# Optimization experiments

Measured on AMD Instinct MI355X. Metric: run time of the kernel, lower is better.

## Reference

```python
import jax, jax.numpy as jnp
import numpy as np

STRIPE = 8
EPS = 1e-5  # PyTorch BatchNorm default eps


def setup_inputs() -> dict:
    key = jax.random.key(0)
    ks = jax.random.split(key, 8)
    b, c, t, h, w = 4, 256, 8, 128, 64
    ic = c // 2  # inter_channels default = in_channels // 2
    scale = 0.02
    return {
        "x": jax.random.normal(ks[0], (b, c, t, h, w), jnp.float32),
        # 1x1 Conv3d weights are just channel-mixing matrices (out, in)
        "g_w": jax.random.normal(ks[1], (ic, c), jnp.float32) * scale,
        "g_b": jnp.zeros((ic,), jnp.float32),
        "theta_w": jax.random.normal(ks[2], (ic, c), jnp.float32) * scale,
        "theta_b": jnp.zeros((ic,), jnp.float32),
        "phi_w": jax.random.normal(ks[3], (ic, c), jnp.float32) * scale,
        "phi_b": jnp.zeros((ic,), jnp.float32),
        "W_w": jax.random.normal(ks[4], (c, ic), jnp.float32) * scale,
        "W_b": jnp.zeros((c,), jnp.float32),
        # BatchNorm3d (eval mode): original inits gamma=beta=0; use nonzero
        # gamma here so the reference output is non-trivial.
        "bn_gamma": jax.random.normal(ks[5], (c,), jnp.float32) * 0.1,
        "bn_beta": jax.random.normal(ks[6], (c,), jnp.float32) * 0.1,
        "bn_mean": jnp.zeros((c,), jnp.float32),
        "bn_var": jnp.ones((c,), jnp.float32),
    }


def reference(x, g_w, g_b, theta_w, theta_b, phi_w, phi_b,
              W_w, W_b, bn_gamma, bn_beta, bn_mean, bn_var):
    b, c, t, h, w = x.shape
    hs = h // STRIPE
    # stripe mean-pool: AdaptiveAvgPool2d(1) over each (hs, w) stripe region
    xr = x.reshape(b, c, t, STRIPE, hs, w)
    d = xr.mean(axis=(4, 5))                      # (b, c, t, stripe)
    S = t * STRIPE
    dn = d.reshape(b, c, S)                       # tokens: (b, c, S)
    # 1x1 conv3d projections == channel matmuls
    g = jnp.einsum('bcs,ic->bsi', dn, g_w) + g_b          # (b, S, ic)
    th = jnp.einsum('bcs,ic->bsi', dn, theta_w) + theta_b  # (b, S, ic)
    ph = jnp.einsum('bcs,ic->bsi', dn, phi_w) + phi_b      # (b, S, ic)
    # small self-attention over stripe tokens
    f = jnp.einsum('bsi,bri->bsr', th, ph)                 # (b, S, S)
    attn = jax.nn.softmax(f, axis=-1)                      # instance='soft'
    y = jnp.einsum('bsr,bri->bsi', attn, g)                # (b, S, ic)
    # output 1x1 conv + BatchNorm3d (eval mode, running stats)
    Wy = jnp.einsum('bsi,ci->bcs', y, W_w) + W_b[None, :, None]  # (b, c, S)
    inv = bn_gamma / jnp.sqrt(bn_var + EPS)
    Wy = (Wy - bn_mean[None, :, None]) * inv[None, :, None] + bn_beta[None, :, None]
    # broadcast each stripe value back over its (hs, w) region + residual
    Wy = Wy.reshape(b, c, t, STRIPE, 1, 1)
    z = (xr + Wy).reshape(b, c, t, h, w)
    return z
```

## Files before the change

### kernel.cpp

```cpp
#include <hip/hip_runtime.h>
#include <hip/hip_bf16.h>
#include <math.h>

#define B 4
#define C 256
#define T 8
#define H 128
#define WW 64
#define IC 128
#define S 64
#define NSTRIPE 8
#define HS 16
#define REGION 1024
#define EPS 1e-5f

__global__ void pool_kernel(const float* __restrict__ x, float* __restrict__ dn) {
    int sb = blockIdx.x;
    const float4* xr = (const float4*)(x + (size_t)sb * REGION);
    float4 v = xr[threadIdx.x];
    float sum = v.x + v.y + v.z + v.w;
    #pragma unroll
    for (int off = 32; off > 0; off >>= 1)
        sum += __shfl_down(sum, off, 64);
    __shared__ float ws[4];
    int wid = threadIdx.x >> 6;
    int lane = threadIdx.x & 63;
    if (lane == 0) ws[wid] = sum;
    __syncthreads();
    if (threadIdx.x == 0) {
        float tot = ws[0] + ws[1] + ws[2] + ws[3];
        dn[sb] = tot * (1.0f / (float)REGION);
    }
}

__global__ void proj_kernel(const float* __restrict__ dn,
                            const float* __restrict__ gw, const float* __restrict__ gb,
                            const float* __restrict__ tw, const float* __restrict__ tb,
                            const float* __restrict__ pw, const float* __restrict__ pb,
                            float* __restrict__ g, float* __restrict__ th,
                            float* __restrict__ ph) {
    int blk = blockIdx.x;
    int b = blk >> 6, s = blk & 63;
    __shared__ float dloc[C];
    for (int ch = threadIdx.x; ch < C; ch += blockDim.x)
        dloc[ch] = dn[(b * C + ch) * S + s];
    __syncthreads();
    int i = threadIdx.x;
    float ag = gb[i], at = tb[i], ap = pb[i];
    const float* gwr = gw + i * C;
    const float* twr = tw + i * C;
    const float* pwr = pw + i * C;
    for (int ch = 0; ch < C; ++ch) {
        float d = dloc[ch];
        ag = fmaf(d, gwr[ch], ag);
        at = fmaf(d, twr[ch], at);
        ap = fmaf(d, pwr[ch], ap);
    }
    size_t o = ((size_t)(b * S + s)) * IC + i;
    g[o] = ag; th[o] = at; ph[o] = ap;
}

__global__ void attn_kernel(const float* __restrict__ g,
                            const float* __restrict__ th,
                            const float* __restrict__ ph,
                            float* __restrict__ y) {
    int blk = blockIdx.x;
    int b = blk >> 6, s = blk & 63;
    __shared__ float p[S];
    __shared__ float thloc[IC];
    int tid = threadIdx.x;
    thloc[tid] = th[((size_t)(b * S + s)) * IC + tid];
    __syncthreads();
    if (tid < 64) {
        int r = tid;
        const float* phr = ph + ((size_t)(b * S + r)) * IC;
        float f = 0.0f;
        for (int i = 0; i < IC; ++i) f = fmaf(thloc[i], phr[i], f);
        float m = f;
        #pragma unroll
        for (int off = 32; off > 0; off >>= 1)
            m = fmaxf(m, __shfl_xor(m, off, 64));
        float e = __expf(f - m);
        float sum = e;
        #pragma unroll
        for (int off = 32; off > 0; off >>= 1)
            sum += __shfl_xor(sum, off, 64);
        p[r] = e / sum;
    }
    __syncthreads();
    int i = tid;
    float acc = 0.0f;
    for (int r = 0; r < S; ++r)
        acc = fmaf(p[r], g[((size_t)(b * S + r)) * IC + i], acc);
    y[((size_t)(b * S + s)) * IC + i] = acc;
}

__global__ void outproj_kernel(const float* __restrict__ y,
                               const float* __restrict__ Ww, const float* __restrict__ Wb,
                               const float* __restrict__ gamma, const float* __restrict__ beta,
                               const float* __restrict__ mean, const float* __restrict__ var,
                               float* __restrict__ wy) {
    int idx = blockIdx.x * blockDim.x + threadIdx.x;
    int s = idx & 63;
    int ch = (idx >> 6) & 255;
    int b = idx >> 14;
    const float* yr = y + ((size_t)(b * S + s)) * IC;
    const float* wr = Ww + (size_t)ch * IC;
    float acc = Wb[ch];
    for (int i = 0; i < IC; ++i) acc = fmaf(yr[i], wr[i], acc);
    float inv = gamma[ch] * rsqrtf(var[ch] + EPS);
    wy[idx] = (acc - mean[ch]) * inv + beta[ch];
}

__global__ void add_kernel(const float* __restrict__ x,
                           const float* __restrict__ wy,
                           float* __restrict__ out) {
    size_t f = (size_t)blockIdx.x * blockDim.x + threadIdx.x;
    const float4* x4 = (const float4*)x;
    float4* o4 = (float4*)out;
    float4 v = x4[f];
    float a = wy[f >> 8];
    v.x += a; v.y += a; v.z += a; v.w += a;
    o4[f] = v;
}

extern "C" void kernel_launch(void* const* d_in, const int* in_sizes, int n_in,
                              void* d_out, int out_size, void* d_ws, size_t ws_size,
                              hipStream_t stream) {
    const float* x       = (const float*)d_in[0];
    const float* g_w     = (const float*)d_in[1];
    const float* g_b     = (const float*)d_in[2];
    const float* theta_w = (const float*)d_in[3];
    const float* theta_b = (const float*)d_in[4];
    const float* phi_w   = (const float*)d_in[5];
    const float* phi_b   = (const float*)d_in[6];
    const float* W_w     = (const float*)d_in[7];
    const float* W_b     = (const float*)d_in[8];
    const float* bn_g    = (const float*)d_in[9];
    const float* bn_b    = (const float*)d_in[10];
    const float* bn_m    = (const float*)d_in[11];
    const float* bn_v    = (const float*)d_in[12];
    float* out = (float*)d_out;

    float* ws = (float*)d_ws;
    float* dn = ws;
    float* g  = dn + B * C * S;
    float* th = g  + B * S * IC;
    float* ph = th + B * S * IC;
    float* y  = ph + B * S * IC;
    float* wy = y  + B * S * IC;

    const int nRegions = B * C * T * NSTRIPE;
    pool_kernel<<<nRegions, 256, 0, stream>>>(x, dn);

    proj_kernel<<<B * S, IC, 0, stream>>>(dn, g_w, g_b, theta_w, theta_b,
                                          phi_w, phi_b, g, th, ph);

    attn_kernel<<<B * S, IC, 0, stream>>>(g, th, ph, y);

    outproj_kernel<<<(B * C * S) / 256, 256, 0, stream>>>(y, W_w, W_b,
                                                          bn_g, bn_b, bn_m, bn_v, wy);

    const size_t nVec4 = (size_t)B * C * T * H * WW / 4;
    add_kernel<<<(int)(nVec4 / 256), 256, 0, stream>>>(x, wy, out);
}
```

Measured before the change: 516.3 us.

## Transpose weights for coalesced projections, fuse attention with output projection

Adds a kernel that transposes the projection weights so that threads in the projection and output-projection loops read consecutive addresses. The pool kernel now reduces 16 regions per wave and writes the pooled tokens transposed, so the projection kernel can load them contiguously. The attention kernel computes scores with wave-parallel dot products and is fused with the output projection and BatchNorm, which removes one launch and the intermediate y buffer. The cost is an extra transpose launch on every call and fewer pool blocks; the large add pass is unchanged and likely dominates the runtime.

```diff
diff --git a/kernel.cpp b/kernel.cpp
--- a/kernel.cpp
+++ b/kernel.cpp
@@ -9,73 +9,111 @@
 #define WW 64
 #define IC 128
 #define S 64
-#define NSTRIPE 8
-#define HS 16
 #define REGION 1024
+#define NREGION 65536
 #define EPS 1e-5f
 
-__global__ void pool_kernel(const float* __restrict__ x, float* __restrict__ dn) {
-    int sb = blockIdx.x;
-    const float4* xr = (const float4*)(x + (size_t)sb * REGION);
-    float4 v = xr[threadIdx.x];
-    float sum = v.x + v.y + v.z + v.w;
-    #pragma unroll
-    for (int off = 32; off > 0; off >>= 1)
-        sum += __shfl_down(sum, off, 64);
-    __shared__ float ws[4];
-    int wid = threadIdx.x >> 6;
-    int lane = threadIdx.x & 63;
-    if (lane == 0) ws[wid] = sum;
-    __syncthreads();
-    if (threadIdx.x == 0) {
-        float tot = ws[0] + ws[1] + ws[2] + ws[3];
-        dn[sb] = tot * (1.0f / (float)REGION);
-    }
-}
-
-__global__ void proj_kernel(const float* __restrict__ dn,
-                            const float* __restrict__ gw, const float* __restrict__ gb,
-                            const float* __restrict__ tw, const float* __restrict__ tb,
-                            const float* __restrict__ pw, const float* __restrict__ pb,
+__global__ void transpose_kernel(const float* __restrict__ gw,
+                                 const float* __restrict__ tw,
+                                 const float* __restrict__ pw,
+                                 const float* __restrict__ Ww,
+                                 float* __restrict__ gwT, float* __restrict__ twT,
+                                 float* __restrict__ pwT, float* __restrict__ WwT) {
+    int t = blockIdx.x * blockDim.x + threadIdx.x;
+    int m = t >> 15;
+    int e = t & 32767;
+    if (m < 3) {
+        int ch = e >> 7, i = e & 127;
+        const float* src = (m == 0) ? gw : (m == 1) ? tw : pw;
+        float* dst = (m == 0) ? gwT : (m == 1) ? twT : pwT;
+        dst[e] = src[i * C + ch];
+    } else {
+        int i = e >> 8, ch = e & 255;
+        WwT[e] = Ww[ch * IC + i];
+    }
+}
+
+__global__ void pool_kernel(const float* __restrict__ x, float* __restrict__ dnT) {
+    int tid = threadIdx.x;
+    int lane = tid & 63;
+    int wgid = (blockIdx.x << 2) | (tid >> 6);
+    int r0 = wgid << 4;
+    for (int k = 0; k < 16; ++k) {
+        int r = r0 + k;
+        const float4* xr = (const float4*)(x + (size_t)r * REGION);
+        float4 a = xr[lane];
+        float4 b = xr[lane + 64];
+        float4 c = xr[lane + 128];
+        float4 d = xr[lane + 192];
+        float sum = (a.x + a.y + a.z + a.w) + (b.x + b.y + b.z + b.w)
+                  + (c.x + c.y + c.z + c.w) + (d.x + d.y + d.z + d.w);
+        #pragma unroll
+        for (int off = 32; off > 0; off >>= 1)
+            sum += __shfl_xor(sum, off, 64);
+        if (lane == 0) {
+            int idx = (r & 0xC000) | ((r & 63) << 8) | ((r >> 6) & 255);
+            dnT[idx] = sum * (1.0f / (float)REGION);
+        }
+    }
+}
+
+__global__ void proj_kernel(const float* __restrict__ dnT,
+                            const float* __restrict__ gwT, const float* __restrict__ gb,
+                            const float* __restrict__ twT, const float* __restrict__ tb,
+                            const float* __restrict__ pwT, const float* __restrict__ pb,
                             float* __restrict__ g, float* __restrict__ th,
                             float* __restrict__ ph) {
     int blk = blockIdx.x;
-    int b = blk >> 6, s = blk & 63;
     __shared__ float dloc[C];
-    for (int ch = threadIdx.x; ch < C; ch += blockDim.x)
-        dloc[ch] = dn[(b * C + ch) * S + s];
+    const float2* dr = (const float2*)(dnT + (size_t)blk * C);
+    ((float2*)dloc)[threadIdx.x] = dr[threadIdx.x];
     __syncthreads();
     int i = threadIdx.x;
     float ag = gb[i], at = tb[i], ap = pb[i];
-    const float* gwr = gw + i * C;
-    const float* twr = tw + i * C;
-    const float* pwr = pw + i * C;
+    #pragma unroll 4
     for (int ch = 0; ch < C; ++ch) {
         float d = dloc[ch];
-        ag = fmaf(d, gwr[ch], ag);
-        at = fmaf(d, twr[ch], at);
-        ap = fmaf(d, pwr[ch], ap);
-    }
-    size_t o = ((size_t)(b * S + s)) * IC + i;
+        int o = (ch << 7) + i;
+        ag = fmaf(d, gwT[o], ag);
+        at = fmaf(d, twT[o], at);
+        ap = fmaf(d, pwT[o], ap);
+    }
+    size_t o = ((size_t)blk) * IC + i;
     g[o] = ag; th[o] = at; ph[o] = ap;
 }
 
-__global__ void attn_kernel(const float* __restrict__ g,
-                            const float* __restrict__ th,
-                            const float* __restrict__ ph,
-                            float* __restrict__ y) {
+__global__ void attn_out_kernel(const float* __restrict__ g,
+                                const float* __restrict__ th,
+                                const float* __restrict__ ph,
+                                const float* __restrict__ WwT,
+                                const float* __restrict__ Wb,
+                                const float* __restrict__ gamma,
+                                const float* __restrict__ beta,
+                                const float* __restrict__ mean,
+                                const float* __restrict__ var,
+                                float* __restrict__ wy) {
     int blk = blockIdx.x;
     int b = blk >> 6, s = blk & 63;
+    int tid = threadIdx.x;
+    int wave = tid >> 6, lane = tid & 63;
+    __shared__ float thloc[IC];
     __shared__ float p[S];
-    __shared__ float thloc[IC];
-    int tid = threadIdx.x;
-    thloc[tid] = th[((size_t)(b * S + s)) * IC + tid];
+    __shared__ float yl[IC];
+    if (tid < IC) thloc[tid] = th[((size_t)blk) * IC + tid];
+    __syncthreads();
+    for (int k = 0; k < 16; ++k) {
+        int r = (wave << 4) + k;
+        const float* phr = ph + ((size_t)(b * S + r)) * IC;
+        float v = thloc[lane] * phr[lane];
+        v = fmaf(thloc[lane + 64], phr[lane + 64], v);
+        #pragma unroll
+        for (int off = 32; off > 0; off >>= 1)
+            v += __shfl_xor(v, off, 64);
+        if (lane == 0) p[r] = v;
+    }
     __syncthreads();
     if (tid < 64) {
-        int r = tid;
-        const float* phr = ph + ((size_t)(b * S + r)) * IC;
-        float f = 0.0f;
-        for (int i = 0; i < IC; ++i) f = fmaf(thloc[i], phr[i], f);
+        float f = p[tid];
         float m = f;
         #pragma unroll
         for (int off = 32; off > 0; off >>= 1)
@@ -85,31 +123,24 @@
         #pragma unroll
         for (int off = 32; off > 0; off >>= 1)
             sum += __shfl_xor(sum, off, 64);
-        p[r] = e / sum;
-    }
-    __syncthreads();
-    int i = tid;
-    float acc = 0.0f;
-    for (int r = 0; r < S; ++r)
-        acc = fmaf(p[r], g[((size_t)(b * S + r)) * IC + i], acc);
-    y[((size_t)(b * S + s)) * IC + i] = acc;
-}
-
-__global__ void outproj_kernel(const float* __restrict__ y,
-                               const float* __restrict__ Ww, const float* __restrict__ Wb,
-                               const float* __restrict__ gamma, const float* __restrict__ beta,
-                               const float* __restrict__ mean, const float* __restrict__ var,
-                               float* __restrict__ wy) {
-    int idx = blockIdx.x * blockDim.x + threadIdx.x;
-    int s = idx & 63;
-    int ch = (idx >> 6) & 255;
-    int b = idx >> 14;
-    const float* yr = y + ((size_t)(b * S + s)) * IC;
-    const float* wr = Ww + (size_t)ch * IC;
+        p[tid] = e / sum;
+    }
+    __syncthreads();
+    if (tid < IC) {
+        float acc = 0.0f;
+        #pragma unroll 4
+        for (int r = 0; r < S; ++r)
+            acc = fmaf(p[r], g[((size_t)(b * S + r)) * IC + tid], acc);
+        yl[tid] = acc;
+    }
+    __syncthreads();
+    int ch = tid;
     float acc = Wb[ch];
-    for (int i = 0; i < IC; ++i) acc = fmaf(yr[i], wr[i], acc);
+    #pragma unroll 4
+    for (int i = 0; i < IC; ++i)
+        acc = fmaf(yl[i], WwT[(i << 8) + ch], acc);
     float inv = gamma[ch] * rsqrtf(var[ch] + EPS);
-    wy[idx] = (acc - mean[ch]) * inv + beta[ch];
+    wy[((size_t)(b * C + ch)) * S + s] = (acc - mean[ch]) * inv + beta[ch];
 }
 
 __global__ void add_kernel(const float* __restrict__ x,
@@ -142,24 +173,27 @@
     const float* bn_v    = (const float*)d_in[12];
     float* out = (float*)d_out;
 
-    float* ws = (float*)d_ws;
-    float* dn = ws;
-    float* g  = dn + B * C * S;
-    float* th = g  + B * S * IC;
-    float* ph = th + B * S * IC;
-    float* y  = ph + B * S * IC;
-    float* wy = y  + B * S * IC;
-
-    const int nRegions = B * C * T * NSTRIPE;
-    pool_kernel<<<nRegions, 256, 0, stream>>>(x, dn);
-
-    proj_kernel<<<B * S, IC, 0, stream>>>(dn, g_w, g_b, theta_w, theta_b,
-                                          phi_w, phi_b, g, th, ph);
-
-    attn_kernel<<<B * S, IC, 0, stream>>>(g, th, ph, y);
-
-    outproj_kernel<<<(B * C * S) / 256, 256, 0, stream>>>(y, W_w, W_b,
-                                                          bn_g, bn_b, bn_m, bn_v, wy);
+    float* ws  = (float*)d_ws;
+    float* dnT = ws;
+    float* gwT = dnT + B * S * C;
+    float* twT = gwT + C * IC;
+    float* pwT = twT + C * IC;
+    float* WwT = pwT + C * IC;
+    float* g   = WwT + C * IC;
+    float* th  = g   + B * S * IC;
+    float* ph  = th  + B * S * IC;
+    float* wy  = ph  + B * S * IC;
+
+    transpose_kernel<<<512, 256, 0, stream>>>(g_w, theta_w, phi_w, W_w,
+                                              gwT, twT, pwT, WwT);
+
+    pool_kernel<<<1024, 256, 0, stream>>>(x, dnT);
+
+    proj_kernel<<<B * S, IC, 0, stream>>>(dnT, gwT, g_b, twT, theta_b,
+                                          pwT, phi_b, g, th, ph);
+
+    attn_out_kernel<<<B * S, 256, 0, stream>>>(g, th, ph, WwT, W_b,
+                                               bn_g, bn_b, bn_m, bn_v, wy);
 
     const size_t nVec4 = (size_t)B * C * T * H * WW / 4;
     add_kernel<<<(int)(nVec4 / 256), 256, 0, stream>>>(x, wy, out);
```

Result: slower. 565.2 us (+9.5%).
